# Kernel tuning notes

Measured on AMD Instinct MI355X. Metric: run time of the kernel, lower is better.

## Reference

```python
import jax, jax.numpy as jnp
import numpy as np

N = 32768       # total nodes across the batch of graphs
E = 524288      # total edges
D = 512         # feature dim (dimensions = [512, 512, 512])
G = 512         # number of graphs (64 nodes each)


def setup_inputs() -> dict:
    key = jax.random.key(0)
    ks = jax.random.split(key, 16)
    inp = {
        'feat': jax.random.normal(ks[0], (N, D), jnp.float32),
        'src': jax.random.randint(ks[1], (E,), 0, N, jnp.int32),
        'dst': jax.random.randint(ks[2], (E,), 0, N, jnp.int32),
        'adj_vals': jax.random.uniform(ks[3], (E,), jnp.float32),
        'graph_ids': (jnp.arange(N, dtype=jnp.int32) // (N // G)),
        'W0': jax.random.normal(ks[4], (D, D), jnp.float32) * 0.05,
        'b0': jnp.zeros((D,), jnp.float32),
        'W1': jax.random.normal(ks[5], (D, D), jnp.float32) * 0.05,
        'b1': jnp.zeros((D,), jnp.float32),
        'gW1': jax.random.normal(ks[6], (D, D), jnp.float32) * 0.05,
        'gb1': jnp.zeros((D,), jnp.float32),
        'gW2': jax.random.normal(ks[7], (D, D), jnp.float32) * 0.05,
        'gb2': jnp.zeros((D,), jnp.float32),
        'gW3': jax.random.normal(ks[8], (D, D), jnp.float32) * 0.05,
        'gb3': jnp.zeros((D,), jnp.float32),
        'gWs': jax.random.normal(ks[9], (D, D), jnp.float32) * 0.05,
        'gbs': jnp.zeros((D,), jnp.float32),
    }
    return inp


def reference(feat, src, dst, adj_vals, graph_ids,
              W0, b0, W1, b1,
              gW1, gb1, gW2, gb2, gW3, gb3, gWs, gbs):
    # GCN layer: act(A_hat @ (X W) + b), A_hat given as weighted edge list
    def gcn(h, W, b, act):
        support = h @ W                              # [N, D]
        msg = adj_vals[:, None] * support[src]       # [E, D]
        agg = jax.ops.segment_sum(msg, dst, num_segments=N)
        return act(agg + b)

    h = gcn(feat, W0, b0, jax.nn.relu)               # hidden layer, act=relu
    h = gcn(h, W1, b1, lambda x: x)                  # last layer, identity act

    # pooling: per-graph mean readout -> sigmoid -> repeat-expand back to nodes
    ones = jnp.ones((N, 1), h.dtype)
    counts = jax.ops.segment_sum(ones, graph_ids, num_segments=G)   # [G, 1]
    pooled = jax.ops.segment_sum(h, graph_ids, num_segments=G) / counts
    g = jax.nn.sigmoid(pooled)[graph_ids]            # [N, D] repeat-expanded

    z = jax.nn.relu(g @ gW1 + gb1)
    z = jax.nn.relu(z @ gW2 + gb2)
    z = jax.nn.relu(z @ gW3 + gb3)
    return z + (g @ gWs + gbs)
```

## Files before the change

kernel.cpp:

```cpp
#include <hip/hip_runtime.h>

typedef unsigned int u32;
typedef unsigned short u16;

typedef __attribute__((ext_vector_type(8))) __bf16 bf16x8;
typedef __attribute__((ext_vector_type(4))) float f32x4;
typedef __attribute__((ext_vector_type(2))) float f32x2;
typedef __attribute__((ext_vector_type(4))) u32 u32x4;

#define N_NODES 32768
#define N_EDGES 524288
#define DIM 512
#define N_GRAPHS 512
#define ECAP 1536
#define NB_CONV 8192
#define NB_TR 1536

__device__ __forceinline__ u16 f2b(float f) {
  union { float f; u32 u; } v; v.f = f;
  u32 r = v.u + 0x7FFFu + ((v.u >> 16) & 1u);
  return (u16)(r >> 16);
}
__device__ __forceinline__ u32 pack2(float a, float b) {
  return (u32)f2b(a) | ((u32)f2b(b) << 16);
}
__device__ __forceinline__ float blo(u32 u) { union { u32 u; float f; } v; v.u = u << 16; return v.f; }
__device__ __forceinline__ float bhi(u32 u) { union { u32 u; float f; } v; v.u = u & 0xFFFF0000u; return v.f; }
__device__ __forceinline__ float b2f(u16 u) { union { u32 u; float f; } v; v.u = ((u32)u) << 16; return v.f; }

__device__ __forceinline__ void async16(const void* g, void* l) {
  __builtin_amdgcn_global_load_lds(
      (const __attribute__((address_space(1))) u32*)g,
      (__attribute__((address_space(3))) u32*)l, 16, 0, 0);
}

__device__ __forceinline__ void acc8(f32x2* a, u32x4 raw, float v) {
  f32x2 v2 = {v, v};
  a[0] += v2 * f32x2{blo(raw.x), bhi(raw.x)};
  a[1] += v2 * f32x2{blo(raw.y), bhi(raw.y)};
  a[2] += v2 * f32x2{blo(raw.z), bhi(raw.z)};
  a[3] += v2 * f32x2{blo(raw.w), bhi(raw.w)};
}

struct WPack {
  const float* src[6];
  u16* dst[6];
};
__global__ __launch_bounds__(256)
void k_prep(const float* __restrict__ feat, u16* __restrict__ featb, WPack wp,
            const int* __restrict__ dstv, int* __restrict__ counts) {
  __shared__ float tile[32][33];
  const int bid = blockIdx.x, tid = threadIdx.x;
  if (bid < NB_CONV) {
    int i = bid * 256 + tid;
    const float4* p = (const float4*)feat;
    float4 a = p[2 * i], b = p[2 * i + 1];
    uint4 o;
    o.x = pack2(a.x, a.y); o.y = pack2(a.z, a.w);
    o.z = pack2(b.x, b.y); o.w = pack2(b.z, b.w);
    ((uint4*)featb)[i] = o;
  } else if (bid < NB_CONV + NB_TR) {
    int idx = bid - NB_CONV;
    int bz = idx >> 8, rem = idx & 255, by = rem >> 4, bx = rem & 15;
    const float* W = wp.src[bz];
    u16* Wt = wp.dst[bz];
    int tx = tid & 31, ty = tid >> 5;
    int bx32 = bx * 32, by32 = by * 32;
    #pragma unroll
    for (int i = 0; i < 4; i++)
      tile[ty + 8 * i][tx] = W[(size_t)(by32 + ty + 8 * i) * DIM + bx32 + tx];
    __syncthreads();
    #pragma unroll
    for (int i = 0; i < 4; i++)
      Wt[(size_t)(bx32 + ty + 8 * i) * DIM + by32 + tx] = f2b(tile[tx][ty + 8 * i]);
  } else {
    int i = (bid - NB_CONV - NB_TR) * 256 + tid;
    atomicAdd(&counts[dstv[i]], 1);
  }
}

__global__ void k_scan(const int* __restrict__ counts, int* __restrict__ offsets,
                       int* __restrict__ cursor) {
  __shared__ int part[1024];
  int t = threadIdx.x;
  const int4* c4 = (const int4*)counts;
  int4 cv[8];
  #pragma unroll
  for (int j = 0; j < 8; j++) cv[j] = c4[t * 8 + j];
  int loc[32];
  int s = 0;
  #pragma unroll
  for (int j = 0; j < 8; j++) {
    loc[4 * j + 0] = s; s += cv[j].x;
    loc[4 * j + 1] = s; s += cv[j].y;
    loc[4 * j + 2] = s; s += cv[j].z;
    loc[4 * j + 3] = s; s += cv[j].w;
  }
  part[t] = s;
  __syncthreads();
  for (int off = 1; off < 1024; off <<= 1) {
    int v = (t >= off) ? part[t - off] : 0;
    __syncthreads();
    part[t] += v;
    __syncthreads();
  }
  int excl = (t == 0) ? 0 : part[t - 1];
  #pragma unroll
  for (int j = 0; j < 8; j++) {
    int4 o = make_int4(excl + loc[4 * j], excl + loc[4 * j + 1],
                       excl + loc[4 * j + 2], excl + loc[4 * j + 3]);
    ((int4*)offsets)[t * 8 + j] = o;
    ((int4*)cursor)[t * 8 + j] = o;
  }
  if (t == 1023) offsets[N_NODES] = excl + s;
}

__global__ void k_fill(const int* __restrict__ src, const int* __restrict__ dst,
                       const float* __restrict__ vals, int* __restrict__ cursor,
                       int2* __restrict__ epack) {
  int i = blockIdx.x * 256 + threadIdx.x;
  if (i >= N_EDGES) return;
  int d = dst[i];
  int p = atomicAdd(&cursor[d], 1);
  epack[p] = make_int2(src[i], __float_as_int(vals[i]));
}

__global__ __launch_bounds__(256)
void k_gemm_bt(const u16* __restrict__ A, const u16* __restrict__ Bt,
               u16* __restrict__ Cout, int M, int Nout, int K) {
  __shared__ __align__(16) u16 As[128 * 32];
  __shared__ __align__(16) u16 Bs[128 * 32];
  const int tid = threadIdx.x;
  const int l = tid & 63;
  const int w = tid >> 6;
  const int mBase = blockIdx.x * 128;
  const int nBase = blockIdx.y * 128;
  const int wm = (w >> 1) * 64;
  const int wn = (w & 1) * 64;
  const int lrow = l >> 2;
  const int lcol = (l & 3) * 8;
  const int q = l >> 4;
  const int r = l & 15;
  f32x4 acc[4][4] = {};

  for (int k0 = 0; k0 < K; k0 += 32) {
    #pragma unroll
    for (int p = 0; p < 2; p++) {
      int row = w * 32 + p * 16 + lrow;
      async16(A + (size_t)(mBase + row) * K + k0 + lcol, (char*)As + w * 2048 + p * 1024);
      async16(Bt + (size_t)(nBase + row) * K + k0 + lcol, (char*)Bs + w * 2048 + p * 1024);
    }
    __syncthreads();
    bf16x8 af[4], bfr[4];
    #pragma unroll
    for (int i = 0; i < 4; i++) af[i] = *(const bf16x8*)&As[(wm + i * 16 + r) * 32 + q * 8];
    #pragma unroll
    for (int j = 0; j < 4; j++) bfr[j] = *(const bf16x8*)&Bs[(wn + j * 16 + r) * 32 + q * 8];
    #pragma unroll
    for (int i = 0; i < 4; i++)
      #pragma unroll
      for (int j = 0; j < 4; j++)
        acc[i][j] = __builtin_amdgcn_mfma_f32_16x16x32_bf16(af[i], bfr[j], acc[i][j], 0, 0, 0);
    __syncthreads();
  }

  #pragma unroll
  for (int i = 0; i < 4; i++) {
    #pragma unroll
    for (int j = 0; j < 4; j++) {
      int col = nBase + wn + j * 16 + r;
      #pragma unroll
      for (int reg = 0; reg < 4; reg++) {
        int rowg = mBase + wm + i * 16 + q * 4 + reg;
        Cout[(size_t)rowg * Nout + col] = f2b(acc[i][j][reg]);
      }
    }
  }
}

template <bool RELU, bool ADDEND, bool OUTF32, bool SIGMOID>
__global__ __launch_bounds__(256)
void k_gemm_small(const u16* __restrict__ A, const u16* __restrict__ Bt,
                  const float* __restrict__ bias, const u16* __restrict__ addend,
                  void* __restrict__ Cout, int Nout, int K) {
  __shared__ __align__(16) u16 As[64 * 32];
  __shared__ __align__(16) u16 Bs[64 * 32];
  const int tid = threadIdx.x;
  const int l = tid & 63;
  const int w = tid >> 6;
  const int mBase = blockIdx.x * 64;
  const int nBase = blockIdx.y * 64;
  const int wm = (w >> 1) * 32;
  const int wn = (w & 1) * 32;
  const int lrow = tid >> 2;
  const int lcol = (tid & 3) * 8;
  const int q = l >> 4;
  const int r = l & 15;
  f32x4 acc[2][2] = {};

  for (int k0 = 0; k0 < K; k0 += 32) {
    async16(A + (size_t)(mBase + lrow) * K + k0 + lcol, (char*)As + tid * 16);
    async16(Bt + (size_t)(nBase + lrow) * K + k0 + lcol, (char*)Bs + tid * 16);
    __syncthreads();
    bf16x8 af[2], bfr[2];
    #pragma unroll
    for (int i = 0; i < 2; i++) af[i] = *(const bf16x8*)&As[(wm + i * 16 + r) * 32 + q * 8];
    #pragma unroll
    for (int j = 0; j < 2; j++) bfr[j] = *(const bf16x8*)&Bs[(wn + j * 16 + r) * 32 + q * 8];
    #pragma unroll
    for (int i = 0; i < 2; i++)
      #pragma unroll
      for (int j = 0; j < 2; j++)
        acc[i][j] = __builtin_amdgcn_mfma_f32_16x16x32_bf16(af[i], bfr[j], acc[i][j], 0, 0, 0);
    __syncthreads();
  }

  #pragma unroll
  for (int i = 0; i < 2; i++) {
    #pragma unroll
    for (int j = 0; j < 2; j++) {
      int col = nBase + wn + j * 16 + r;
      float bv = bias[col];
      #pragma unroll
      for (int reg = 0; reg < 4; reg++) {
        int rowg = mBase + wm + i * 16 + q * 4 + reg;
        float v = acc[i][j][reg] + bv;
        if (ADDEND) v += b2f(addend[(size_t)rowg * Nout + col]);
        if (RELU) v = fmaxf(v, 0.0f);
        if (SIGMOID) v = 1.0f / (1.0f + expf(-v));
        if (OUTF32) ((float*)Cout)[(size_t)rowg * Nout + col] = v;
        else ((u16*)Cout)[(size_t)rowg * Nout + col] = f2b(v);
      }
    }
  }
}

template <bool RELU, bool POOL>
__global__ __launch_bounds__(256)
void k_agg(const u16* __restrict__ support, const int* __restrict__ offsets,
           const int2* __restrict__ epack, const float* __restrict__ bias,
           u16* __restrict__ outp) {
  __shared__ int2 eLds[ECAP];
  __shared__ float poolLds[4][64];
  const int chunk = blockIdx.x & 7;
  const int cidx  = blockIdx.x >> 3;
  const int rowBase = cidx * 64;
  const int e0b = offsets[rowBase];
  const int nb = offsets[rowBase + 64] - e0b;
  for (int i = threadIdx.x; i < min(nb, ECAP); i += 256)
    eLds[i] = epack[e0b + i];
  __syncthreads();

  const int wi = threadIdx.x >> 6;
  const int l  = threadIdx.x & 63;
  const int grp = l >> 3;
  const int li  = l & 7;
  const int colOff = chunk * 64 + li * 8;
  const u16* spc = support + colOff;

  f32x2 b[4] = {};
  if (!POOL) {
    const float4* bp = (const float4*)(bias + colOff);
    float4 x = bp[0], y = bp[1];
    b[0] = f32x2{x.x, x.y}; b[1] = f32x2{x.z, x.w};
    b[2] = f32x2{y.x, y.y}; b[3] = f32x2{y.z, y.w};
  }

  f32x2 psum[4] = {};

  #pragma unroll
  for (int pass = 0; pass < 2; pass++) {
    int r = rowBase + wi * 16 + pass * 8 + grp;
    int re0 = offsets[r] - e0b;
    int deg = offsets[r + 1] - e0b - re0;

    f32x2 a[4] = {b[0], b[1], b[2], b[3]};

    if (nb <= ECAP) {
      int i = 0;
      for (; i + 4 <= deg; i += 4) {
        int2 p0 = eLds[re0 + i];
        int2 p1 = eLds[re0 + i + 1];
        int2 p2 = eLds[re0 + i + 2];
        int2 p3 = eLds[re0 + i + 3];
        u32x4 r0 = *(const u32x4*)(spc + (size_t)p0.x * DIM);
        u32x4 r1 = *(const u32x4*)(spc + (size_t)p1.x * DIM);
        u32x4 r2 = *(const u32x4*)(spc + (size_t)p2.x * DIM);
        u32x4 r3 = *(const u32x4*)(spc + (size_t)p3.x * DIM);
        acc8(a, r0, __int_as_float(p0.y));
        acc8(a, r1, __int_as_float(p1.y));
        acc8(a, r2, __int_as_float(p2.y));
        acc8(a, r3, __int_as_float(p3.y));
      }
      for (; i < deg; i++) {
        int2 p = eLds[re0 + i];
        u32x4 raw = *(const u32x4*)(spc + (size_t)p.x * DIM);
        acc8(a, raw, __int_as_float(p.y));
      }
    } else {
      for (int i = 0; i < deg; i++) {
        int gi = re0 + i;
        int2 p = (gi < ECAP) ? eLds[gi] : epack[e0b + gi];
        u32x4 raw = *(const u32x4*)(spc + (size_t)p.x * DIM);
        acc8(a, raw, __int_as_float(p.y));
      }
    }

    if (POOL) {
      #pragma unroll
      for (int i = 0; i < 4; i++) psum[i] += a[i];
    } else {
      if (RELU) {
        #pragma unroll
        for (int i = 0; i < 4; i++) {
          a[i].x = fmaxf(a[i].x, 0.0f);
          a[i].y = fmaxf(a[i].y, 0.0f);
        }
      }
      u32x4 o;
      o.x = pack2(a[0].x, a[0].y); o.y = pack2(a[1].x, a[1].y);
      o.z = pack2(a[2].x, a[2].y); o.w = pack2(a[3].x, a[3].y);
      *(u32x4*)(outp + (size_t)r * DIM + colOff) = o;
    }
  }

  if (POOL) {
    #pragma unroll
    for (int k = 0; k < 4; k++) {
      psum[k].x += __shfl_xor(psum[k].x, 8);  psum[k].y += __shfl_xor(psum[k].y, 8);
      psum[k].x += __shfl_xor(psum[k].x, 16); psum[k].y += __shfl_xor(psum[k].y, 16);
      psum[k].x += __shfl_xor(psum[k].x, 32); psum[k].y += __shfl_xor(psum[k].y, 32);
    }
    if (grp == 0) {
      #pragma unroll
      for (int k = 0; k < 4; k++) {
        poolLds[wi][li * 8 + 2 * k]     = psum[k].x;
        poolLds[wi][li * 8 + 2 * k + 1] = psum[k].y;
      }
    }
    __syncthreads();
    if (threadIdx.x < 64) {
      int cc = threadIdx.x;
      float s = poolLds[0][cc] + poolLds[1][cc] + poolLds[2][cc] + poolLds[3][cc];
      outp[(size_t)cidx * DIM + chunk * 64 + cc] = f2b(s * (1.0f / 64.0f));
    }
  }
}

__global__ void k_expand(const float* __restrict__ small, float* __restrict__ out) {
  int i = blockIdx.x * 256 + threadIdx.x;
  int col4 = i & 127;
  int node = i >> 7;
  float4 v = ((const float4*)small)[((node >> 6) << 7) + col4];
  ((float4*)out)[i] = v;
}

extern "C" void kernel_launch(void* const* d_in, const int* in_sizes, int n_in,
                              void* d_out, int out_size, void* d_ws, size_t ws_size,
                              hipStream_t stream) {
  const float* feat = (const float*)d_in[0];
  const int* src    = (const int*)d_in[1];
  const int* dst    = (const int*)d_in[2];
  const float* adj  = (const float*)d_in[3];
  const float* W0  = (const float*)d_in[5];
  const float* b0  = (const float*)d_in[6];
  const float* W1  = (const float*)d_in[7];
  const float* b1  = (const float*)d_in[8];
  const float* gW1 = (const float*)d_in[9];
  const float* gb1 = (const float*)d_in[10];
  const float* gW2 = (const float*)d_in[11];
  const float* gb2 = (const float*)d_in[12];
  const float* gW3 = (const float*)d_in[13];
  const float* gb3 = (const float*)d_in[14];
  const float* gWs = (const float*)d_in[15];
  const float* gbs = (const float*)d_in[16];

  char* ws = (char*)d_ws;
  size_t off = 0;
  auto alloc = [&](size_t bytes) -> void* {
    void* p = ws + off;
    off = (off + bytes + 255) & ~(size_t)255;
    return p;
  };
  u16* bufA = (u16*)alloc((size_t)N_NODES * DIM * 2);
  u16* bufB = (u16*)alloc((size_t)N_NODES * DIM * 2);
  u16* wt[6];
  for (int i = 0; i < 6; i++) wt[i] = (u16*)alloc((size_t)DIM * DIM * 2);
  int* counts   = (int*)alloc((size_t)N_NODES * 4);
  int* offsets  = (int*)alloc((size_t)(N_NODES + 1) * 4);
  int* cursor   = (int*)alloc((size_t)N_NODES * 4);
  int2* epack   = (int2*)alloc((size_t)N_EDGES * 8);
  u16* qb       = (u16*)alloc((size_t)N_GRAPHS * DIM * 2);
  u16* gfeat    = (u16*)alloc((size_t)N_GRAPHS * DIM * 2);
  u16* z1       = (u16*)alloc((size_t)N_GRAPHS * DIM * 2);
  u16* z2       = (u16*)alloc((size_t)N_GRAPHS * DIM * 2);
  u16* z3       = (u16*)alloc((size_t)N_GRAPHS * DIM * 2);
  float* osmall = (float*)alloc((size_t)N_GRAPHS * DIM * 4);

  (void)hipMemsetAsync(counts, 0, (size_t)N_NODES * 4, stream);

  WPack wp;
  wp.src[0] = W0; wp.src[1] = W1; wp.src[2] = gW1; wp.src[3] = gW2; wp.src[4] = gW3; wp.src[5] = gWs;
  for (int i = 0; i < 6; i++) wp.dst[i] = wt[i];

  k_prep<<<NB_CONV + NB_TR + N_EDGES / 256, 256, 0, stream>>>(feat, bufA, wp, dst, counts);
  k_scan<<<1, 1024, 0, stream>>>(counts, offsets, cursor);
  k_fill<<<N_EDGES / 256, 256, 0, stream>>>(src, dst, adj, cursor, epack);

  k_gemm_bt<<<dim3(N_NODES / 128, DIM / 128), 256, 0, stream>>>(bufA, wt[0], bufB, N_NODES, DIM, DIM);
  k_agg<true, false><<<4096, 256, 0, stream>>>(bufB, offsets, epack, b0, bufA);
  k_agg<false, true><<<4096, 256, 0, stream>>>(bufA, offsets, epack, nullptr, qb);
  k_gemm_small<false, false, false, true><<<dim3(8, 8), 256, 0, stream>>>(qb, wt[1], b1, nullptr, gfeat, DIM, DIM);

  k_gemm_small<true, false, false, false><<<dim3(8, 8), 256, 0, stream>>>(gfeat, wt[2], gb1, nullptr, z1, DIM, DIM);
  k_gemm_small<true, false, false, false><<<dim3(8, 8), 256, 0, stream>>>(z1, wt[3], gb2, nullptr, z2, DIM, DIM);
  k_gemm_small<true, false, false, false><<<dim3(8, 8), 256, 0, stream>>>(z2, wt[4], gb3, nullptr, z3, DIM, DIM);
  k_gemm_small<false, true, true, false><<<dim3(8, 8), 256, 0, stream>>>(gfeat, wt[5], gbs, z3, osmall, DIM, DIM);

  k_expand<<<(N_NODES * DIM / 4) / 256, 256, 0, stream>>>(osmall, (float*)d_out);
}
```

Before: 390.6 us.

## Fuse feature bf16 conversion into GEMM, fuse FF chain, deepen agg unroll

Three changes. The fp32 to bf16 conversion of the node features is folded into the first GEMM's A-tile load, which removes a separate pass and the bf16 copy of the features. The five small per-graph GEMMs are merged into one kernel of 32 blocks that keeps 16-row activations in LDS between stages, which removes four launches and the round trips of the intermediates through global memory. The aggregation inner loop gains an 8-wide unrolled gather for more loads in flight. The A loads in the GEMM become synchronous global reads instead of async copies to LDS, and the fused FF kernel uses only 32 blocks and reads weights straight from global memory, so it has little parallelism.

Result: slower. 504.5 us (+29.1%).

```diff
diff --git a/kernel.cpp b/kernel.cpp
--- a/kernel.cpp
+++ b/kernel.cpp
@@ -13,8 +13,9 @@
 #define DIM 512
 #define N_GRAPHS 512
 #define ECAP 1536
-#define NB_CONV 8192
 #define NB_TR 1536
+
+#define MFMA16 __builtin_amdgcn_mfma_f32_16x16x32_bf16
 
 __device__ __forceinline__ u16 f2b(float f) {
   union { float f; u32 u; } v; v.f = f;
@@ -47,21 +48,11 @@
   u16* dst[6];
 };
 __global__ __launch_bounds__(256)
-void k_prep(const float* __restrict__ feat, u16* __restrict__ featb, WPack wp,
-            const int* __restrict__ dstv, int* __restrict__ counts) {
+void k_prep(WPack wp, const int* __restrict__ dstv, int* __restrict__ counts) {
   __shared__ float tile[32][33];
   const int bid = blockIdx.x, tid = threadIdx.x;
-  if (bid < NB_CONV) {
-    int i = bid * 256 + tid;
-    const float4* p = (const float4*)feat;
-    float4 a = p[2 * i], b = p[2 * i + 1];
-    uint4 o;
-    o.x = pack2(a.x, a.y); o.y = pack2(a.z, a.w);
-    o.z = pack2(b.x, b.y); o.w = pack2(b.z, b.w);
-    ((uint4*)featb)[i] = o;
-  } else if (bid < NB_CONV + NB_TR) {
-    int idx = bid - NB_CONV;
-    int bz = idx >> 8, rem = idx & 255, by = rem >> 4, bx = rem & 15;
+  if (bid < NB_TR) {
+    int bz = bid >> 8, rem = bid & 255, by = rem >> 4, bx = rem & 15;
     const float* W = wp.src[bz];
     u16* Wt = wp.dst[bz];
     int tx = tid & 31, ty = tid >> 5;
@@ -74,7 +65,7 @@
     for (int i = 0; i < 4; i++)
       Wt[(size_t)(bx32 + ty + 8 * i) * DIM + by32 + tx] = f2b(tile[tx][ty + 8 * i]);
   } else {
-    int i = (bid - NB_CONV - NB_TR) * 256 + tid;
+    int i = (bid - NB_TR) * 256 + tid;
     atomicAdd(&counts[dstv[i]], 1);
   }
 }
@@ -126,7 +117,7 @@
 }
 
 __global__ __launch_bounds__(256)
-void k_gemm_bt(const u16* __restrict__ A, const u16* __restrict__ Bt,
+void k_gemm_bt(const float* __restrict__ Af, const u16* __restrict__ Bt,
                u16* __restrict__ Cout, int M, int Nout, int K) {
   __shared__ __align__(16) u16 As[128 * 32];
   __shared__ __align__(16) u16 Bs[128 * 32];
@@ -147,8 +138,13 @@
     #pragma unroll
     for (int p = 0; p < 2; p++) {
       int row = w * 32 + p * 16 + lrow;
-      async16(A + (size_t)(mBase + row) * K + k0 + lcol, (char*)As + w * 2048 + p * 1024);
+      const float4* fp = (const float4*)(Af + (size_t)(mBase + row) * K + k0 + lcol);
+      float4 x = fp[0], y = fp[1];
       async16(Bt + (size_t)(nBase + row) * K + k0 + lcol, (char*)Bs + w * 2048 + p * 1024);
+      uint4 o;
+      o.x = pack2(x.x, x.y); o.y = pack2(x.z, x.w);
+      o.z = pack2(y.x, y.y); o.w = pack2(y.z, y.w);
+      *(uint4*)((char*)As + w * 2048 + p * 1024 + l * 16) = o;
     }
     __syncthreads();
     bf16x8 af[4], bfr[4];
@@ -160,7 +156,7 @@
     for (int i = 0; i < 4; i++)
       #pragma unroll
       for (int j = 0; j < 4; j++)
-        acc[i][j] = __builtin_amdgcn_mfma_f32_16x16x32_bf16(af[i], bfr[j], acc[i][j], 0, 0, 0);
+        acc[i][j] = MFMA16(af[i], bfr[j], acc[i][j], 0, 0, 0);
     __syncthreads();
   }
 
@@ -178,61 +174,67 @@
   }
 }
 
-template <bool RELU, bool ADDEND, bool OUTF32, bool SIGMOID>
 __global__ __launch_bounds__(256)
-void k_gemm_small(const u16* __restrict__ A, const u16* __restrict__ Bt,
-                  const float* __restrict__ bias, const u16* __restrict__ addend,
-                  void* __restrict__ Cout, int Nout, int K) {
-  __shared__ __align__(16) u16 As[64 * 32];
-  __shared__ __align__(16) u16 Bs[64 * 32];
+void k_ff(const u16* __restrict__ qb,
+          const u16* __restrict__ w1t, const float* __restrict__ b1,
+          const u16* __restrict__ gw1t, const float* __restrict__ gb1,
+          const u16* __restrict__ gw2t, const float* __restrict__ gb2,
+          const u16* __restrict__ gw3t, const float* __restrict__ gb3,
+          const u16* __restrict__ gwst, const float* __restrict__ gbs,
+          float* __restrict__ osmall) {
+  __shared__ __align__(16) u16 bufX[16 * 520];
+  __shared__ __align__(16) u16 bufY[16 * 520];
+  __shared__ __align__(16) u16 bufG[16 * 520];
   const int tid = threadIdx.x;
   const int l = tid & 63;
   const int w = tid >> 6;
-  const int mBase = blockIdx.x * 64;
-  const int nBase = blockIdx.y * 64;
-  const int wm = (w >> 1) * 32;
-  const int wn = (w & 1) * 32;
-  const int lrow = tid >> 2;
-  const int lcol = (tid & 3) * 8;
   const int q = l >> 4;
   const int r = l & 15;
-  f32x4 acc[2][2] = {};
-
-  for (int k0 = 0; k0 < K; k0 += 32) {
-    async16(A + (size_t)(mBase + lrow) * K + k0 + lcol, (char*)As + tid * 16);
-    async16(Bt + (size_t)(nBase + lrow) * K + k0 + lcol, (char*)Bs + tid * 16);
-    __syncthreads();
-    bf16x8 af[2], bfr[2];
-    #pragma unroll
-    for (int i = 0; i < 2; i++) af[i] = *(const bf16x8*)&As[(wm + i * 16 + r) * 32 + q * 8];
-    #pragma unroll
-    for (int j = 0; j < 2; j++) bfr[j] = *(const bf16x8*)&Bs[(wn + j * 16 + r) * 32 + q * 8];
-    #pragma unroll
-    for (int i = 0; i < 2; i++)
-      #pragma unroll
-      for (int j = 0; j < 2; j++)
-        acc[i][j] = __builtin_amdgcn_mfma_f32_16x16x32_bf16(af[i], bfr[j], acc[i][j], 0, 0, 0);
-    __syncthreads();
-  }
-
-  #pragma unroll
-  for (int i = 0; i < 2; i++) {
-    #pragma unroll
-    for (int j = 0; j < 2; j++) {
-      int col = nBase + wn + j * 16 + r;
+  const int rb = blockIdx.x * 16;
+
+  for (int idx = tid; idx < 16 * 64; idx += 256) {
+    int row = idx >> 6, c8 = (idx & 63) * 8;
+    *(uint4*)&bufX[row * 520 + c8] = *(const uint4*)(qb + (size_t)(rb + row) * DIM + c8);
+  }
+  __syncthreads();
+
+  auto stage = [&](const u16* A, const u16* Wt, const float* bias, int mode,
+                   const u16* addY, u16* dst) {
+    f32x4 acc[8] = {};
+    for (int k0 = 0; k0 < DIM; k0 += 32) {
+      bf16x8 af = *(const bf16x8*)&A[r * 520 + k0 + q * 8];
+      #pragma unroll
+      for (int j = 0; j < 8; j++) {
+        bf16x8 bf = *(const bf16x8*)(Wt + (size_t)(w * 128 + j * 16 + r) * DIM + k0 + q * 8);
+        acc[j] = MFMA16(af, bf, acc[j], 0, 0, 0);
+      }
+    }
+    #pragma unroll
+    for (int j = 0; j < 8; j++) {
+      int col = w * 128 + j * 16 + r;
       float bv = bias[col];
       #pragma unroll
       for (int reg = 0; reg < 4; reg++) {
-        int rowg = mBase + wm + i * 16 + q * 4 + reg;
-        float v = acc[i][j][reg] + bv;
-        if (ADDEND) v += b2f(addend[(size_t)rowg * Nout + col]);
-        if (RELU) v = fmaxf(v, 0.0f);
-        if (SIGMOID) v = 1.0f / (1.0f + expf(-v));
-        if (OUTF32) ((float*)Cout)[(size_t)rowg * Nout + col] = v;
-        else ((u16*)Cout)[(size_t)rowg * Nout + col] = f2b(v);
-      }
-    }
-  }
+        int row = q * 4 + reg;
+        float v = acc[j][reg] + bv;
+        if (mode == 0) v = 1.0f / (1.0f + expf(-v));
+        else if (mode == 1) v = fmaxf(v, 0.0f);
+        else {
+          v += b2f(addY[row * 520 + col]);
+          osmall[(size_t)(rb + row) * DIM + col] = v;
+          continue;
+        }
+        dst[row * 520 + col] = f2b(v);
+      }
+    }
+    __syncthreads();
+  };
+
+  stage(bufX, w1t,  b1,  0, nullptr, bufG);
+  stage(bufG, gw1t, gb1, 1, nullptr, bufY);
+  stage(bufY, gw2t, gb2, 1, nullptr, bufX);
+  stage(bufX, gw3t, gb3, 1, nullptr, bufY);
+  stage(bufG, gwst, gbs, 2, bufY,    nullptr);
 }
 
 template <bool RELU, bool POOL>
@@ -278,11 +280,19 @@
 
     if (nb <= ECAP) {
       int i = 0;
+      for (; i + 8 <= deg; i += 8) {
+        int2 p[8];
+        u32x4 rr[8];
+        #pragma unroll
+        for (int u = 0; u < 8; u++) p[u] = eLds[re0 + i + u];
+        #pragma unroll
+        for (int u = 0; u < 8; u++) rr[u] = *(const u32x4*)(spc + (size_t)p[u].x * DIM);
+        #pragma unroll
+        for (int u = 0; u < 8; u++) acc8(a, rr[u], __int_as_float(p[u].y));
+      }
       for (; i + 4 <= deg; i += 4) {
-        int2 p0 = eLds[re0 + i];
-        int2 p1 = eLds[re0 + i + 1];
-        int2 p2 = eLds[re0 + i + 2];
-        int2 p3 = eLds[re0 + i + 3];
+        int2 p0 = eLds[re0 + i], p1 = eLds[re0 + i + 1];
+        int2 p2 = eLds[re0 + i + 2], p3 = eLds[re0 + i + 3];
         u32x4 r0 = *(const u32x4*)(spc + (size_t)p0.x * DIM);
         u32x4 r1 = *(const u32x4*)(spc + (size_t)p1.x * DIM);
         u32x4 r2 = *(const u32x4*)(spc + (size_t)p2.x * DIM);
@@ -391,10 +401,6 @@
   int* cursor   = (int*)alloc((size_t)N_NODES * 4);
   int2* epack   = (int2*)alloc((size_t)N_EDGES * 8);
   u16* qb       = (u16*)alloc((size_t)N_GRAPHS * DIM * 2);
-  u16* gfeat    = (u16*)alloc((size_t)N_GRAPHS * DIM * 2);
-  u16* z1       = (u16*)alloc((size_t)N_GRAPHS * DIM * 2);
-  u16* z2       = (u16*)alloc((size_t)N_GRAPHS * DIM * 2);
-  u16* z3       = (u16*)alloc((size_t)N_GRAPHS * DIM * 2);
   float* osmall = (float*)alloc((size_t)N_GRAPHS * DIM * 4);
 
   (void)hipMemsetAsync(counts, 0, (size_t)N_NODES * 4, stream);
@@ -403,19 +409,14 @@
   wp.src[0] = W0; wp.src[1] = W1; wp.src[2] = gW1; wp.src[3] = gW2; wp.src[4] = gW3; wp.src[5] = gWs;
   for (int i = 0; i < 6; i++) wp.dst[i] = wt[i];
 
-  k_prep<<<NB_CONV + NB_TR + N_EDGES / 256, 256, 0, stream>>>(feat, bufA, wp, dst, counts);
+  k_prep<<<NB_TR + N_EDGES / 256, 256, 0, stream>>>(wp, dst, counts);
   k_scan<<<1, 1024, 0, stream>>>(counts, offsets, cursor);
   k_fill<<<N_EDGES / 256, 256, 0, stream>>>(src, dst, adj, cursor, epack);
 
-  k_gemm_bt<<<dim3(N_NODES / 128, DIM / 128), 256, 0, stream>>>(bufA, wt[0], bufB, N_NODES, DIM, DIM);
+  k_gemm_bt<<<dim3(N_NODES / 128, DIM / 128), 256, 0, stream>>>(feat, wt[0], bufB, N_NODES, DIM, DIM);
   k_agg<true, false><<<4096, 256, 0, stream>>>(bufB, offsets, epack, b0, bufA);
   k_agg<false, true><<<4096, 256, 0, stream>>>(bufA, offsets, epack, nullptr, qb);
-  k_gemm_small<false, false, false, true><<<dim3(8, 8), 256, 0, stream>>>(qb, wt[1], b1, nullptr, gfeat, DIM, DIM);
-
-  k_gemm_small<true, false, false, false><<<dim3(8, 8), 256, 0, stream>>>(gfeat, wt[2], gb1, nullptr, z1, DIM, DIM);
-  k_gemm_small<true, false, false, false><<<dim3(8, 8), 256, 0, stream>>>(z1, wt[3], gb2, nullptr, z2, DIM, DIM);
-  k_gemm_small<true, false, false, false><<<dim3(8, 8), 256, 0, stream>>>(z2, wt[4], gb3, nullptr, z3, DIM, DIM);
-  k_gemm_small<false, true, true, false><<<dim3(8, 8), 256, 0, stream>>>(gfeat, wt[5], gbs, z3, osmall, DIM, DIM);
+  k_ff<<<32, 256, 0, stream>>>(qb, wt[1], b1, wt[2], gb1, wt[3], gb2, wt[4], gb3, wt[5], gbs, osmall);
 
   k_expand<<<(N_NODES * DIM / 4) / 256, 256, 0, stream>>>(osmall, (float*)d_out);
 }
```
